# Optimization experiments

Measured on AMD Instinct MI355X. Metric: run time of the kernel, lower is better.

## Reference

```python
import jax, jax.numpy as jnp
import numpy as np
import math

D = 256; B = 4; N = 2048; IN = 16; POS = 3; LAT = 128
DEPTH = 3; RATIO = 0.5; NBLK = 8  # depth*2 + 2 final blocks


def _silu(x):
    return x * jax.nn.sigmoid(x)


def _ln(h, g, b):
    m = h.mean(-1, keepdims=True)
    v = h.var(-1, keepdims=True)  # biased, matches nn.LayerNorm
    return (h - m) / jnp.sqrt(v + 1e-5) * g + b


def _block(h, A, g, b, w1, b1, w2, b2, eps):
    # h: (B, n, D), A: (B, n, n) binary adjacency (block-diag equivalent)
    hn = _ln(h, g, b)
    nb = jnp.einsum('bij,bjd->bid', A, hn)  # sparse.mm(adj, h) per graph
    t = (1.0 + eps) * hn + nb
    t = _silu(t @ w1 + b1) @ w2 + b2
    return h + t


def _forward(x, adj, pos, in_w, in_b, pw1, pb1, pw2, pb2,
             bg, bb, bw1, bb1, bw2, bb2, beps, pool_p, lw, lb, batch_size):
    Bsz = batch_size
    n = adj.shape[0]
    d = in_w.shape[1]
    h = x @ in_w + in_b  # (B*N, D)
    # positional embedding: tile, normalize (unbiased std like torch), MLP
    pt = jnp.tile(pos, (Bsz, 1))
    pn = (pt - pt.mean(0, keepdims=True)) / (pt.std(0, ddof=1, keepdims=True) + 1e-8)
    pe = _silu(pn @ pw1 + pb1) @ pw2 + pb2
    h = (h + pe).reshape(Bsz, n, d)
    A = jnp.broadcast_to(adj, (Bsz, n, n))  # shared block-diag tiles
    blk = 0
    for dep in range(DEPTH):
        for _ in range(2):  # blocks_per_stage
            h = _block(h, A, bg[blk], bb[blk], bw1[blk], bb1[blk],
                       bw2[blk], bb2[blk], beps[blk])
            blk += 1
        # TopKPool: projection score, per-graph top-k, tanh gating
        p = pool_p[dep]
        score = h @ p / jnp.linalg.norm(p)  # (B, n)
        k = int(math.ceil(RATIO * h.shape[1]))  # static
        idx = jnp.sort(jax.lax.top_k(score, k)[1], axis=-1)  # (B, k)
        gate = jnp.tanh(jnp.take_along_axis(score, idx, axis=1))
        h = jnp.take_along_axis(h, idx[:, :, None], axis=1) * gate[:, :, None]
        # subgraph_coo + to_binary: adj[idx][:, idx] per graph
        A = jax.vmap(lambda a, i: a[i][:, i])(A, idx)
        A = (A > 0).astype(h.dtype)
    for _ in range(2):  # final_stage
        h = _block(h, A, bg[blk], bb[blk], bw1[blk], bb1[blk],
                   bw2[blk], bb2[blk], beps[blk])
        blk += 1
    hm = h.mean(1)
    hs = h.std(1, ddof=1) + 1e-6  # torch .std is unbiased
    return jnp.concatenate([hm, hs], axis=-1) @ lw + lb  # (B, LAT)


def setup_inputs() -> dict:
    key = jax.random.key(0)
    ks = jax.random.split(key, 12)
    f32 = jnp.float32
    s = 1.0 / np.sqrt(D)
    x = jax.random.normal(ks[0], (B * N, IN), f32)
    adj = (jax.random.uniform(ks[1], (N, N)) < 0.004).astype(f32)  # ~8 nbrs/node
    pos = jax.random.normal(ks[2], (N, POS), f32)
    return {
        'x': x, 'adj': adj, 'pos': pos,
        'in_w': jax.random.normal(ks[3], (IN, D), f32) / np.sqrt(IN),
        'in_b': jnp.zeros(D, f32),
        'pw1': jax.random.normal(ks[4], (POS, D), f32) / np.sqrt(POS),
        'pb1': jnp.zeros(D, f32),
        'pw2': jax.random.normal(ks[5], (D, D), f32) * s,
        'pb2': jnp.zeros(D, f32),
        'bg': jnp.ones((NBLK, D), f32),
        'bb': jnp.zeros((NBLK, D), f32),
        'bw1': jax.random.normal(ks[6], (NBLK, D, D), f32) * s,
        'bb1': jnp.zeros((NBLK, D), f32),
        'bw2': jax.random.normal(ks[7], (NBLK, D, D), f32) * (0.5 * s),
        'bb2': jnp.zeros((NBLK, D), f32),
        'beps': jnp.zeros(NBLK, f32),
        'pool_p': jax.random.normal(ks[8], (DEPTH, D), f32) * s,
        'lw': jax.random.normal(ks[9], (2 * D, LAT), f32) / np.sqrt(2 * D),
        'lb': jnp.zeros(LAT, f32),
        'batch_size': B,
    }


def reference(x, adj, pos, in_w, in_b, pw1, pb1, pw2, pb2,
              bg, bb, bw1, bb1, bw2, bb2, beps, pool_p, lw, lb, batch_size):
    return _forward(x, adj, pos, in_w, in_b, pw1, pb1, pw2, pb2,
                    bg, bb, bw1, bb1, bw2, bb2, beps, pool_p, lw, lb, batch_size)
```

## Files before the change

kernel.cpp:

```cpp
#include <hip/hip_runtime.h>
#include <hip/hip_bf16.h>

#define NTOT 2048
#define DD 256
#define BSZ 4

typedef _Float16 half_t;
typedef __attribute__((ext_vector_type(8))) _Float16 halfx8;
typedef __attribute__((ext_vector_type(4))) _Float16 halfx4;
typedef __attribute__((ext_vector_type(4))) float f32x4;

__device__ __forceinline__ float blockReduceSum256(float v) {
    __shared__ float red[4];
    for (int off = 32; off > 0; off >>= 1) v += __shfl_down(v, off);
    int lane = threadIdx.x & 63, w = threadIdx.x >> 6;
    __syncthreads();
    if (lane == 0) red[w] = v;
    __syncthreads();
    return red[0] + red[1] + red[2] + red[3];
}

#define SB_WPREP 4352
#define SB_STAT  4356
#define SB_A2L   4868
#define SB_MAPS  4900
__global__ void __launch_bounds__(256) setup_kernel(
    const float* __restrict__ bw1, const float* __restrict__ bw2,
    const float* __restrict__ pw2, half_t* __restrict__ Wt,
    const float* __restrict__ pos, float* __restrict__ pstats,
    const float* __restrict__ poolp, float* __restrict__ pinv,
    const float* __restrict__ adj, int* __restrict__ ldeg0, int* __restrict__ lcol0,
    int* __restrict__ orig, int* __restrict__ inv) {
    int bid = blockIdx.x, tid = threadIdx.x;
    if (bid < SB_WPREP) {
        int m = bid >> 8, rem = bid & 255;
        int nb = (rem >> 4) * 16, kb = (rem & 15) * 16;
        const float* W = (m < 8) ? (bw1 + (size_t)m * DD * DD)
                      : (m < 16) ? (bw2 + (size_t)(m - 8) * DD * DD)
                                 : pw2;
        __shared__ float s[16][17];
        int i = tid >> 4, j = tid & 15;
        s[i][j] = W[(size_t)(kb + i) * DD + nb + j];
        __syncthreads();
        Wt[(size_t)m * DD * DD + (size_t)(nb + i) * DD + kb + j] = (half_t)s[j][i];
    } else if (bid < SB_STAT) {
        int which = bid - SB_WPREP;
        if (which == 0) {
            float s[3] = {0.f, 0.f, 0.f};
            for (int i = tid; i < NTOT; i += 256)
                for (int c = 0; c < 3; ++c) s[c] += pos[i * 3 + c];
            float m[3];
            for (int c = 0; c < 3; ++c) m[c] = blockReduceSum256(s[c]) / (float)NTOT;
            float q[3] = {0.f, 0.f, 0.f};
            for (int i = tid; i < NTOT; i += 256)
                for (int c = 0; c < 3; ++c) { float d = pos[i * 3 + c] - m[c]; q[c] += d * d; }
            for (int c = 0; c < 3; ++c) {
                float t = blockReduceSum256(q[c]);
                if (tid == 0) {
                    float var = ((float)BSZ * t) / ((float)BSZ * NTOT - 1.0f);
                    pstats[c] = m[c];
                    pstats[3 + c] = 1.0f / (sqrtf(var) + 1e-8f);
                }
            }
        } else {
            int dep = which - 1;
            float v = poolp[dep * DD + tid];
            float ss = blockReduceSum256(v * v);
            if (tid == 0) pinv[dep] = rsqrtf(ss);
        }
    } else if (bid < SB_A2L) {
        int row = (bid - SB_STAT) * 4 + (tid >> 6);
        int lane = tid & 63;
        int run = 0;
        for (int j0 = 0; j0 < NTOT; j0 += 64) {
            int j = j0 + lane;
            bool pred = adj[(size_t)row * NTOT + j] != 0.f;
            unsigned long long mask = __ballot(pred);
            if (pred) {
                int pos2 = run + __popcll(mask & ((1ull << lane) - 1ull));
                if (pos2 < 64) lcol0[row * 64 + pos2] = j;
            }
            run += __popcll(mask);
        }
        if (lane == 0) ldeg0[row] = run < 64 ? run : 64;
    } else {
        int t = (bid - SB_A2L) * 256 + tid;
        int i = t & (NTOT - 1);
        orig[t] = i; inv[t] = i;
    }
}

__global__ void __launch_bounds__(256) pe_h_kernel(
    const float* __restrict__ pos, const float* __restrict__ pstats,
    const float* __restrict__ pw1, const float* __restrict__ pb1,
    const half_t* __restrict__ Wt16, const float* __restrict__ pb2,
    const float* __restrict__ x, const float* __restrict__ in_w,
    const float* __restrict__ in_b, float* __restrict__ h, float* __restrict__ z) {
    __shared__ half_t tb[16][264];
    __shared__ float iw[16][DD];
    __shared__ float xs[16][16];
    __shared__ float part[4][16][2];
    __shared__ float mrs[16][2];
    int tid = threadIdx.x;
    int i0 = blockIdx.x * 16;
    {
        int rl = tid >> 4, cb = (tid & 15) * 16;
        float pn[3];
#pragma unroll
        for (int c = 0; c < 3; ++c)
            pn[c] = (pos[(i0 + rl) * 3 + c] - pstats[c]) * pstats[3 + c];
#pragma unroll
        for (int u = 0; u < 16; ++u) {
            int d = cb + u;
            float a = pb1[d];
            a += pn[0] * pw1[d];
            a += pn[1] * pw1[DD + d];
            a += pn[2] * pw1[2 * DD + d];
            a = a / (1.0f + expf(-a));
            tb[rl][d] = (half_t)a;
        }
        int k = tid >> 4;
#pragma unroll
        for (int u = 0; u < 16; ++u) iw[k][cb + u] = in_w[k * DD + cb + u];
    }
    __syncthreads();
    int w = tid >> 6, l = tid & 63;
    int lo = l & 15, hi = l >> 4;
    int kb = hi * 8;
    float pe_r[4][4];
    {
        f32x4 acc[4] = {};
#pragma unroll
        for (int k0 = 0; k0 < DD; k0 += 32) {
            halfx8 a0 = *(const halfx8*)&tb[lo][kb + k0];
#pragma unroll
            for (int j = 0; j < 4; ++j) {
                halfx8 bj = *(const halfx8*)(Wt16 + (size_t)(w * 64 + j * 16 + lo) * DD + kb + k0);
                acc[j] = __builtin_amdgcn_mfma_f32_16x16x32_f16(a0, bj, acc[j], 0, 0, 0);
            }
        }
#pragma unroll
        for (int j = 0; j < 4; ++j) {
            float bs = pb2[w * 64 + j * 16 + lo];
#pragma unroll
            for (int q = 0; q < 4; ++q) pe_r[j][q] = acc[j][q] + bs;
        }
    }
    float xb[4];
#pragma unroll
    for (int j = 0; j < 4; ++j) xb[j] = in_b[w * 64 + j * 16 + lo];
    for (int b = 0; b < BSZ; ++b) {
        __syncthreads();
        xs[tid >> 4][tid & 15] = x[(size_t)(b * NTOT + i0 + (tid >> 4)) * 16 + (tid & 15)];
        __syncthreads();
        float vh[4][4];
#pragma unroll
        for (int q = 0; q < 4; ++q) {
            int rl = hi * 4 + q;
            float s = 0.f, ss = 0.f;
#pragma unroll
            for (int j = 0; j < 4; ++j) {
                int c = w * 64 + j * 16 + lo;
                float acc = xb[j];
#pragma unroll
                for (int k = 0; k < 16; ++k) acc += xs[rl][k] * iw[k][c];
                float v = acc + pe_r[j][q];
                vh[j][q] = v;
                s += v; ss += v * v;
            }
#pragma unroll
            for (int m = 1; m < 16; m <<= 1) { s += __shfl_xor(s, m); ss += __shfl_xor(ss, m); }
            if (lo == 0) { part[w][rl][0] = s; part[w][rl][1] = ss; }
        }
        __syncthreads();
        if (tid < 16) {
            float s = 0.f, ss = 0.f;
#pragma unroll
            for (int w2 = 0; w2 < 4; ++w2) { s += part[w2][tid][0]; ss += part[w2][tid][1]; }
            float mean = s * (1.0f / DD);
            float var = ss * (1.0f / DD) - mean * mean;
            mrs[tid][0] = mean;
            mrs[tid][1] = rsqrtf(var + 1e-5f);
        }
        __syncthreads();
#pragma unroll
        for (int q = 0; q < 4; ++q) {
            int rl = hi * 4 + q;
            size_t r = (size_t)(b * NTOT + i0 + rl);
            float mean = mrs[rl][0], rs = mrs[rl][1];
#pragma unroll
            for (int j = 0; j < 4; ++j) {
                int c = w * 64 + j * 16 + lo;
                float v = vh[j][q];
                h[r * DD + c] = v;
                z[r * DD + c] = (v - mean) * rs;
            }
        }
    }
}

template <int SCORE>
__global__ void __launch_bounds__(256) layer_kernel(
    float* __restrict__ h, const float* __restrict__ zin, float* __restrict__ zout,
    const half_t* __restrict__ Wt1, const half_t* __restrict__ Wt2,
    const float* __restrict__ b1v, const float* __restrict__ b2v,
    const float* __restrict__ gv, const float* __restrict__ bbv,
    const float* __restrict__ beps, int blk,
    const int* __restrict__ ldeg0, const int* __restrict__ lcol0,
    const int* __restrict__ orig, const int* __restrict__ inv,
    const float* __restrict__ poolp, const float* __restrict__ pinv_all,
    float* __restrict__ scores, int dep, int n, int tag) {
    __shared__ half_t tb[16][264];
    __shared__ half_t ub[16][264];
    __shared__ float part[4][16][3];
    __shared__ float mrs[16][2];
    int tid = threadIdx.x;
    int rowBase = blockIdx.x * 16;
    float eps1 = 1.0f + beps[blk];

    {
        int rl = tid >> 4, cg = tid & 15;
        int r = rowBase + rl;
        int b = r / n, i = r - b * n;
        const f32x4* zb = (const f32x4*)zin + (size_t)b * n * 64;
        f32x4 acc[4];
#pragma unroll
        for (int u = 0; u < 4; ++u) acc[u] = zb[(size_t)i * 64 + cg + 16 * u] * eps1;
        int cnt = 0;
        if (tag == 0) {
            int deg = ldeg0[i];
            const int* lc = lcol0 + i * 64;
            int p = 0;
            for (; p + 4 <= deg; p += 4) {
                int j0 = lc[p], j1 = lc[p + 1], j2 = lc[p + 2], j3 = lc[p + 3];
#pragma unroll
                for (int u = 0; u < 4; ++u) {
                    f32x4 v0 = zb[(size_t)j0 * 64 + cg + 16 * u];
                    f32x4 v1 = zb[(size_t)j1 * 64 + cg + 16 * u];
                    f32x4 v2 = zb[(size_t)j2 * 64 + cg + 16 * u];
                    f32x4 v3 = zb[(size_t)j3 * 64 + cg + 16 * u];
                    acc[u] += (v0 + v1) + (v2 + v3);
                }
            }
            for (; p < deg; ++p) {
                int j = lc[p];
#pragma unroll
                for (int u = 0; u < 4; ++u) acc[u] += zb[(size_t)j * 64 + cg + 16 * u];
            }
            cnt = deg;
        } else {
            int o = orig[b * NTOT + i];
            int deg = ldeg0[o];
            const int* lc = lcol0 + o * 64;
            const int* invb = inv + b * NTOT;
            int p = 0;
            for (; p + 4 <= deg; p += 4) {
                int c0 = lc[p], c1 = lc[p + 1], c2 = lc[p + 2], c3 = lc[p + 3];
                int v0 = invb[c0], v1 = invb[c1], v2 = invb[c2], v3 = invb[c3];
                if ((v0 >> 12) == tag) {
                    int j = v0 & 4095; ++cnt;
#pragma unroll
                    for (int u = 0; u < 4; ++u) acc[u] += zb[(size_t)j * 64 + cg + 16 * u];
                }
                if ((v1 >> 12) == tag) {
                    int j = v1 & 4095; ++cnt;
#pragma unroll
                    for (int u = 0; u < 4; ++u) acc[u] += zb[(size_t)j * 64 + cg + 16 * u];
                }
                if ((v2 >> 12) == tag) {
                    int j = v2 & 4095; ++cnt;
#pragma unroll
                    for (int u = 0; u < 4; ++u) acc[u] += zb[(size_t)j * 64 + cg + 16 * u];
                }
                if ((v3 >> 12) == tag) {
                    int j = v3 & 4095; ++cnt;
#pragma unroll
                    for (int u = 0; u < 4; ++u) acc[u] += zb[(size_t)j * 64 + cg + 16 * u];
                }
            }
            for (; p < deg; ++p) {
                int v = invb[lc[p]];
                if ((v >> 12) == tag) {
                    int j = v & 4095; ++cnt;
#pragma unroll
                    for (int u = 0; u < 4; ++u) acc[u] += zb[(size_t)j * 64 + cg + 16 * u];
                }
            }
        }
        float coefb = eps1 + (float)cnt;
#pragma unroll
        for (int u = 0; u < 4; ++u) {
            int c4 = cg + 16 * u;
            f32x4 gvv = ((const f32x4*)gv)[c4];
            f32x4 bvv = ((const f32x4*)bbv)[c4];
            f32x4 tv = gvv * acc[u] + bvv * coefb;
            halfx4 th;
#pragma unroll
            for (int e = 0; e < 4; ++e) th[e] = (half_t)tv[e];
            *(halfx4*)&tb[rl][c4 * 4] = th;
        }
    }
    __syncthreads();

    int w = tid >> 6, l = tid & 63;
    int lo = l & 15, hi = l >> 4;
    int kb = hi * 8;

    {
        f32x4 acc[4] = {};
#pragma unroll
        for (int k0 = 0; k0 < DD; k0 += 32) {
            halfx8 a0 = *(const halfx8*)&tb[lo][kb + k0];
#pragma unroll
            for (int j = 0; j < 4; ++j) {
                halfx8 bj = *(const halfx8*)(Wt1 + (size_t)(w * 64 + j * 16 + lo) * DD + kb + k0);
                acc[j] = __builtin_amdgcn_mfma_f32_16x16x32_f16(a0, bj, acc[j], 0, 0, 0);
            }
        }
        float bs[4];
#pragma unroll
        for (int j = 0; j < 4; ++j) bs[j] = b1v[w * 64 + j * 16 + lo];
#pragma unroll
        for (int q = 0; q < 4; ++q)
#pragma unroll
            for (int j = 0; j < 4; ++j) {
                float v = acc[j][q] + bs[j];
                v = v / (1.0f + expf(-v));
                ub[hi * 4 + q][w * 64 + j * 16 + lo] = (half_t)v;
            }
    }
    __syncthreads();

    {
        f32x4 acc[4] = {};
#pragma unroll
        for (int k0 = 0; k0 < DD; k0 += 32) {
            halfx8 a0 = *(const halfx8*)&ub[lo][kb + k0];
#pragma unroll
            for (int j = 0; j < 4; ++j) {
                halfx8 bj = *(const halfx8*)(Wt2 + (size_t)(w * 64 + j * 16 + lo) * DD + kb + k0);
                acc[j] = __builtin_amdgcn_mfma_f32_16x16x32_f16(a0, bj, acc[j], 0, 0, 0);
            }
        }
        float bs[4], pv[4] = {};
#pragma unroll
        for (int j = 0; j < 4; ++j) bs[j] = b2v[w * 64 + j * 16 + lo];
        if (SCORE) {
#pragma unroll
            for (int j = 0; j < 4; ++j) pv[j] = poolp[dep * DD + w * 64 + j * 16 + lo];
        }
        float vh[4][4];
#pragma unroll
        for (int q = 0; q < 4; ++q) {
            int r = rowBase + hi * 4 + q;
            float s = 0.f, ss = 0.f, sp = 0.f;
#pragma unroll
            for (int j = 0; j < 4; ++j) {
                int c = w * 64 + j * 16 + lo;
                float v = h[(size_t)r * DD + c] + acc[j][q] + bs[j];
                vh[j][q] = v;
                s += v; ss += v * v;
                if (SCORE) sp += v * pv[j];
            }
#pragma unroll
            for (int m = 1; m < 16; m <<= 1) {
                s += __shfl_xor(s, m); ss += __shfl_xor(ss, m);
                if (SCORE) sp += __shfl_xor(sp, m);
            }
            if (lo == 0) {
                int rl = hi * 4 + q;
                part[w][rl][0] = s; part[w][rl][1] = ss;
                if (SCORE) part[w][rl][2] = sp;
            }
        }
        __syncthreads();
        if (tid < 16) {
            float s = 0.f, ss = 0.f, sp = 0.f;
#pragma unroll
            for (int w2 = 0; w2 < 4; ++w2) {
                s += part[w2][tid][0]; ss += part[w2][tid][1];
                if (SCORE) sp += part[w2][tid][2];
            }
            float mean = s * (1.0f / DD);
            float var = ss * (1.0f / DD) - mean * mean;
            mrs[tid][0] = mean;
            mrs[tid][1] = rsqrtf(var + 1e-5f);
            if (SCORE) {
                int r = rowBase + tid;
                int b2 = r / n, ii = r - b2 * n;
                scores[b2 * NTOT + ii] = sp * pinv_all[dep];
            }
        }
        __syncthreads();
#pragma unroll
        for (int q = 0; q < 4; ++q) {
            int rl = hi * 4 + q;
            int r = rowBase + rl;
            float mean = mrs[rl][0], rs = mrs[rl][1];
#pragma unroll
            for (int j = 0; j < 4; ++j) {
                int c = w * 64 + j * 16 + lo;
                float v = vh[j][q];
                h[(size_t)r * DD + c] = v;
                zout[(size_t)r * DD + c] = (v - mean) * rs;
            }
        }
    }
}

__global__ void topk_kernel(const float* __restrict__ scores, const int* __restrict__ orig_cur,
                            int* __restrict__ orig_next, int* __restrict__ idx_local,
                            float* __restrict__ gate, int n, int k) {
    __shared__ unsigned keys[2048];
    __shared__ int hist[256];
    __shared__ int sg[256], se[256];
    __shared__ int sh_bucket, sh_r, sh_cnt;
    __shared__ unsigned cand[256];
    __shared__ unsigned sh_thr;
    int b = blockIdx.x;
    const float* sc = scores + b * NTOT;
    int tid = threadIdx.x;
    for (int i = tid; i < n; i += 256) {
        unsigned u = __float_as_uint(sc[i]);
        keys[i] = (u & 0x80000000u) ? ~u : (u | 0x80000000u);
    }
    hist[tid] = 0;
    if (tid == 0) sh_cnt = 0;
    __syncthreads();
    for (int i = tid; i < n; i += 256) atomicAdd(&hist[keys[i] >> 24], 1);
    __syncthreads();
    int cnt = hist[tid];
    sg[tid] = cnt;
    __syncthreads();
    for (int off = 1; off < 256; off <<= 1) {
        int v = (tid >= off) ? sg[tid - off] : 0;
        __syncthreads();
        sg[tid] += v;
        __syncthreads();
    }
    int r = n - k;
    int incl = sg[tid], excl = incl - cnt;
    if (excl <= r && r < incl) { sh_bucket = tid; sh_r = r - excl; }
    __syncthreads();
    int b1 = sh_bucket, r1 = sh_r;
    int c = hist[b1];
    unsigned thrkey;
    if (c <= 256) {
        for (int i = tid; i < n; i += 256) {
            unsigned key = keys[i];
            if ((key >> 24) == (unsigned)b1) {
                int pos = atomicAdd(&sh_cnt, 1);
                cand[pos] = key;
            }
        }
        __syncthreads();
        if (tid < c) {
            unsigned mine = cand[tid];
            int less = 0, eq = 0;
            for (int j = 0; j < c; ++j) {
                unsigned oth = cand[j];
                less += (oth < mine); eq += (oth == mine);
            }
            if (less <= r1 && r1 < less + eq) sh_thr = mine;
        }
        __syncthreads();
        thrkey = sh_thr;
    } else {
        unsigned prefix = ((unsigned)b1) << 24;
        int rr = r1;
        for (int shift = 16; shift >= 0; shift -= 8) {
            __syncthreads();
            hist[tid] = 0;
            __syncthreads();
            unsigned mask = 0xFFFFFFFFu << (shift + 8);
            for (int i = tid; i < n; i += 256) {
                unsigned key = keys[i];
                if ((key & mask) == (prefix & mask)) atomicAdd(&hist[(key >> shift) & 255], 1);
            }
            __syncthreads();
            int cnt2 = hist[tid];
            sg[tid] = cnt2;
            __syncthreads();
            for (int off = 1; off < 256; off <<= 1) {
                int v = (tid >= off) ? sg[tid - off] : 0;
                __syncthreads();
                sg[tid] += v;
                __syncthreads();
            }
            int incl2 = sg[tid], excl2 = incl2 - cnt2;
            if (excl2 <= rr && rr < incl2) { sh_bucket = tid; sh_r = rr - excl2; }
            __syncthreads();
            prefix |= ((unsigned)sh_bucket) << shift;
            rr = sh_r;
            __syncthreads();
        }
        thrkey = prefix;
    }
    unsigned uthr = (thrkey & 0x80000000u) ? (thrkey ^ 0x80000000u) : ~thrkey;
    float thr = __uint_as_float(uthr);
    int chunk = n / 256;
    int base = tid * chunk;
    int cgt = 0, ceq = 0;
    for (int u = 0; u < chunk; ++u) {
        float s = sc[base + u];
        cgt += (s > thr); ceq += (s == thr);
    }
    sg[tid] = cgt; se[tid] = ceq; __syncthreads();
    for (int off = 1; off < 256; off <<= 1) {
        int vg = (tid >= off) ? sg[tid - off] : 0;
        int ve = (tid >= off) ? se[tid - off] : 0;
        __syncthreads();
        sg[tid] += vg; se[tid] += ve;
        __syncthreads();
    }
    int total_gt = sg[255];
    int ties = k - total_gt;
    int gtb = sg[tid] - cgt, eqb = se[tid] - ceq;
    for (int u = 0; u < chunk; ++u) {
        int i = base + u;
        float s = sc[i];
        bool isgt = (s > thr), iseq = (s == thr);
        bool keep = isgt || (iseq && eqb < ties);
        if (keep) {
            int pos = gtb + (eqb < ties ? eqb : ties);
            idx_local[b * NTOT + pos] = i;
            gate[b * NTOT + pos] = tanhf(s);
            orig_next[b * NTOT + pos] = orig_cur[b * NTOT + i];
        }
        gtb += isgt; eqb += iseq;
    }
}

__global__ void __launch_bounds__(64) gather_kernel(
    const float* __restrict__ h, const int* __restrict__ idx_local,
    const float* __restrict__ gate, const int* __restrict__ orig_new,
    float* __restrict__ hout, float* __restrict__ zout, int* __restrict__ inv,
    int n_old, int k, int tag) {
    int r = blockIdx.x;
    int b = r / k, rr = r - b * k;
    int lane = threadIdx.x;
    int src = idx_local[b * NTOT + rr];
    float gg = gate[b * NTOT + rr];
    f32x4 v = ((const f32x4*)h)[(size_t)(b * n_old + src) * 64 + lane] * gg;
    ((f32x4*)hout)[(size_t)r * 64 + lane] = v;
    float s = v[0] + v[1] + v[2] + v[3];
    float ss = v[0] * v[0] + v[1] * v[1] + v[2] * v[2] + v[3] * v[3];
#pragma unroll
    for (int m = 1; m < 64; m <<= 1) { s += __shfl_xor(s, m); ss += __shfl_xor(ss, m); }
    float mean = s * (1.0f / DD);
    float rs = rsqrtf(ss * (1.0f / DD) - mean * mean + 1e-5f);
    f32x4 zv = (v - mean) * rs;
    ((f32x4*)zout)[(size_t)r * 64 + lane] = zv;
    if (lane == 0) inv[b * NTOT + orig_new[b * NTOT + rr]] = (tag << 12) | rr;
}

__global__ void __launch_bounds__(256) readout_final_kernel(
    const float* __restrict__ h, const float* __restrict__ lw,
    const float* __restrict__ lb, float* __restrict__ out) {
    __shared__ float feat[512];
    int b = blockIdx.x, d = threadIdx.x;
    const float* hb = h + (size_t)b * 256 * DD;
    float s = 0.f;
    for (int i = 0; i < 256; ++i) s += hb[(size_t)i * DD + d];
    float mean = s / 256.0f;
    float s2 = 0.f;
    for (int i = 0; i < 256; ++i) {
        float diff = hb[(size_t)i * DD + d] - mean;
        s2 += diff * diff;
    }
    feat[d] = mean;
    feat[256 + d] = sqrtf(s2 / 255.0f) + 1e-6f;
    __syncthreads();
    if (d < 128) {
        float acc = lb[d];
        for (int k = 0; k < 512; ++k) acc += feat[k] * lw[k * 128 + d];
        out[b * 128 + d] = acc;
    }
}

extern "C" void kernel_launch(void* const* d_in, const int* in_sizes, int n_in,
                              void* d_out, int out_size, void* d_ws, size_t ws_size,
                              hipStream_t stream) {
    (void)in_sizes; (void)n_in; (void)out_size; (void)ws_size;
    const float* x     = (const float*)d_in[0];
    const float* adj   = (const float*)d_in[1];
    const float* pos   = (const float*)d_in[2];
    const float* in_w  = (const float*)d_in[3];
    const float* in_b  = (const float*)d_in[4];
    const float* pw1   = (const float*)d_in[5];
    const float* pb1   = (const float*)d_in[6];
    const float* pw2   = (const float*)d_in[7];
    const float* pb2   = (const float*)d_in[8];
    const float* bg    = (const float*)d_in[9];
    const float* bb    = (const float*)d_in[10];
    const float* bw1   = (const float*)d_in[11];
    const float* bb1   = (const float*)d_in[12];
    const float* bw2   = (const float*)d_in[13];
    const float* bb2   = (const float*)d_in[14];
    const float* beps  = (const float*)d_in[15];
    const float* poolp = (const float*)d_in[16];
    const float* lw    = (const float*)d_in[17];
    const float* lb    = (const float*)d_in[18];
    float* out = (float*)d_out;

    char* wp = (char*)d_ws;
    auto alloc = [&](size_t bytes) -> void* {
        void* p = (void*)wp;
        wp += (bytes + 255) & ~(size_t)255;
        return p;
    };
    const size_t HBYTES = (size_t)BSZ * NTOT * DD * sizeof(float);
    float*  h    = (float*)alloc(HBYTES);
    float*  bufC = (float*)alloc(HBYTES);
    float*  zA   = (float*)alloc(HBYTES);
    float*  zB   = (float*)alloc(HBYTES);
    half_t* Wt   = (half_t*)alloc((size_t)17 * DD * DD * sizeof(half_t));
    float* pstats  = (float*)alloc(8 * sizeof(float));
    float* pinv    = (float*)alloc(4 * sizeof(float));
    float* scores  = (float*)alloc(BSZ * NTOT * sizeof(float));
    float* gate    = (float*)alloc(BSZ * NTOT * sizeof(float));
    int*   origA   = (int*)alloc(BSZ * NTOT * sizeof(int));
    int*   origB   = (int*)alloc(BSZ * NTOT * sizeof(int));
    int*   idxl    = (int*)alloc(BSZ * NTOT * sizeof(int));
    int*   inv     = (int*)alloc(BSZ * NTOT * sizeof(int));
    int*   ldeg0   = (int*)alloc(NTOT * sizeof(int));
    int*   lcol0   = (int*)alloc((size_t)NTOT * 64 * sizeof(int));

    setup_kernel<<<SB_MAPS, 256, 0, stream>>>(bw1, bw2, pw2, Wt, pos, pstats, poolp, pinv,
                                              adj, ldeg0, lcol0, origA, inv);
    pe_h_kernel<<<NTOT / 16, 256, 0, stream>>>(pos, pstats, pw1, pb1,
                                               Wt + (size_t)16 * DD * DD, pb2,
                                               x, in_w, in_b, h, zA);

    float* hcur = h;
    float* halt = bufC;
    float* zin = zA;
    float* zout = zB;
    int* orig = origA;
    int* orign = origB;
    int n = NTOT;
    int blk = 0;
    for (int dep = 0; dep < 4; ++dep) {
        for (int s = 0; s < 2; ++s) {
            int rows = BSZ * n;
            if (s == 1 && dep < 3) {
                layer_kernel<1><<<rows / 16, 256, 0, stream>>>(
                    hcur, zin, zout, Wt + (size_t)blk * DD * DD, Wt + (size_t)(8 + blk) * DD * DD,
                    bb1 + blk * DD, bb2 + blk * DD, bg + blk * DD, bb + blk * DD,
                    beps, blk, ldeg0, lcol0, orig, inv, poolp, pinv, scores, dep, n, dep);
            } else {
                layer_kernel<0><<<rows / 16, 256, 0, stream>>>(
                    hcur, zin, zout, Wt + (size_t)blk * DD * DD, Wt + (size_t)(8 + blk) * DD * DD,
                    bb1 + blk * DD, bb2 + blk * DD, bg + blk * DD, bb + blk * DD,
                    beps, blk, ldeg0, lcol0, orig, inv, nullptr, nullptr, nullptr, 0, n, dep);
            }
            { float* t = zin; zin = zout; zout = t; }
            ++blk;
        }
        if (dep < 3) {
            int k = n / 2;
            topk_kernel<<<BSZ, 256, 0, stream>>>(scores, orig, orign, idxl, gate, n, k);
            { int* t = orig; orig = orign; orign = t; }
            gather_kernel<<<BSZ * k, 64, 0, stream>>>(hcur, idxl, gate, orig, halt, zin, inv,
                                                      n, k, dep + 1);
            { float* t = hcur; hcur = halt; halt = t; }
            n = k;
        }
    }
    readout_final_kernel<<<BSZ, 256, 0, stream>>>(hcur, lw, lb, out);
}
```

Before: 283.3 us.

## Split sparse aggregation from MLP into separate kernels for large stages

For the first two depth stages (larger graphs), the fused layer kernel is replaced by two kernels. A wave-per-row aggregation kernel gathers neighbor rows and writes the LayerNorm-affine result as fp16 to a new buffer, and a separate MFMA MLP kernel reads that buffer. This gives the irregular gather much more parallelism (rows/4 blocks, one row per wave) and removes gather stalls from the GEMM blocks. The cost is an extra launch per layer and an fp16 intermediate round trip through global memory. Smaller later stages keep the fused kernel.

```diff
diff --git a/kernel.cpp b/kernel.cpp
--- a/kernel.cpp
+++ b/kernel.cpp
@@ -199,6 +199,181 @@
     }
 }
 
+__global__ void __launch_bounds__(256) agg_kernel(
+    const float* __restrict__ zin, half_t* __restrict__ tb,
+    const float* __restrict__ gv, const float* __restrict__ bbv,
+    const float* __restrict__ beps, int blk,
+    const int* __restrict__ ldeg0, const int* __restrict__ lcol0,
+    const int* __restrict__ orig, const int* __restrict__ inv, int n, int tag) {
+    int w = threadIdx.x >> 6, lane = threadIdx.x & 63;
+    int r = blockIdx.x * 4 + w;
+    int b = r / n, i = r - b * n;
+    float eps1 = 1.0f + beps[blk];
+    const f32x4* zb = (const f32x4*)zin + (size_t)b * n * 64;
+    f32x4 acc = zb[(size_t)i * 64 + lane] * eps1;
+    int cnt = 0;
+    if (tag == 0) {
+        int deg = ldeg0[i];
+        const int* lc = lcol0 + i * 64;
+        int p = 0;
+        for (; p + 4 <= deg; p += 4) {
+            int j0 = lc[p], j1 = lc[p + 1], j2 = lc[p + 2], j3 = lc[p + 3];
+            f32x4 v0 = zb[(size_t)j0 * 64 + lane];
+            f32x4 v1 = zb[(size_t)j1 * 64 + lane];
+            f32x4 v2 = zb[(size_t)j2 * 64 + lane];
+            f32x4 v3 = zb[(size_t)j3 * 64 + lane];
+            acc += (v0 + v1) + (v2 + v3);
+        }
+        for (; p < deg; ++p) acc += zb[(size_t)lc[p] * 64 + lane];
+        cnt = deg;
+    } else {
+        int o = orig[b * NTOT + i];
+        int deg = ldeg0[o];
+        const int* lc = lcol0 + o * 64;
+        const int* invb = inv + b * NTOT;
+        int p = 0;
+        for (; p + 4 <= deg; p += 4) {
+            int v0 = invb[lc[p]], v1 = invb[lc[p + 1]];
+            int v2 = invb[lc[p + 2]], v3 = invb[lc[p + 3]];
+            if ((v0 >> 12) == tag) { acc += zb[(size_t)(v0 & 4095) * 64 + lane]; ++cnt; }
+            if ((v1 >> 12) == tag) { acc += zb[(size_t)(v1 & 4095) * 64 + lane]; ++cnt; }
+            if ((v2 >> 12) == tag) { acc += zb[(size_t)(v2 & 4095) * 64 + lane]; ++cnt; }
+            if ((v3 >> 12) == tag) { acc += zb[(size_t)(v3 & 4095) * 64 + lane]; ++cnt; }
+        }
+        for (; p < deg; ++p) {
+            int v = invb[lc[p]];
+            if ((v >> 12) == tag) { acc += zb[(size_t)(v & 4095) * 64 + lane]; ++cnt; }
+        }
+    }
+    float coefb = eps1 + (float)cnt;
+    f32x4 gvv = ((const f32x4*)gv)[lane];
+    f32x4 bvv = ((const f32x4*)bbv)[lane];
+    f32x4 tv = gvv * acc + bvv * coefb;
+    halfx4 th;
+#pragma unroll
+    for (int e = 0; e < 4; ++e) th[e] = (half_t)tv[e];
+    ((halfx4*)tb)[(size_t)r * 64 + lane] = th;
+}
+
+template <int SCORE>
+__global__ void __launch_bounds__(256) mlp_kernel(
+    float* __restrict__ h, const half_t* __restrict__ tbg, float* __restrict__ zout,
+    const half_t* __restrict__ Wt1, const half_t* __restrict__ Wt2,
+    const float* __restrict__ b1v, const float* __restrict__ b2v,
+    const float* __restrict__ poolp, const float* __restrict__ pinv_all,
+    float* __restrict__ scores, int dep, int n) {
+    __shared__ half_t ub[16][264];
+    __shared__ float part[4][16][3];
+    __shared__ float mrs[16][2];
+    int tid = threadIdx.x;
+    int rowBase = blockIdx.x * 16;
+    int w = tid >> 6, l = tid & 63;
+    int lo = l & 15, hi = l >> 4;
+    int kb = hi * 8;
+
+    {
+        const half_t* a0p = tbg + (size_t)(rowBase + lo) * DD + kb;
+        f32x4 acc[4] = {};
+#pragma unroll
+        for (int k0 = 0; k0 < DD; k0 += 32) {
+            halfx8 a0 = *(const halfx8*)(a0p + k0);
+#pragma unroll
+            for (int j = 0; j < 4; ++j) {
+                halfx8 bj = *(const halfx8*)(Wt1 + (size_t)(w * 64 + j * 16 + lo) * DD + kb + k0);
+                acc[j] = __builtin_amdgcn_mfma_f32_16x16x32_f16(a0, bj, acc[j], 0, 0, 0);
+            }
+        }
+        float bs[4];
+#pragma unroll
+        for (int j = 0; j < 4; ++j) bs[j] = b1v[w * 64 + j * 16 + lo];
+#pragma unroll
+        for (int q = 0; q < 4; ++q)
+#pragma unroll
+            for (int j = 0; j < 4; ++j) {
+                float v = acc[j][q] + bs[j];
+                v = v / (1.0f + expf(-v));
+                ub[hi * 4 + q][w * 64 + j * 16 + lo] = (half_t)v;
+            }
+    }
+    __syncthreads();
+
+    {
+        f32x4 acc[4] = {};
+#pragma unroll
+        for (int k0 = 0; k0 < DD; k0 += 32) {
+            halfx8 a0 = *(const halfx8*)&ub[lo][kb + k0];
+#pragma unroll
+            for (int j = 0; j < 4; ++j) {
+                halfx8 bj = *(const halfx8*)(Wt2 + (size_t)(w * 64 + j * 16 + lo) * DD + kb + k0);
+                acc[j] = __builtin_amdgcn_mfma_f32_16x16x32_f16(a0, bj, acc[j], 0, 0, 0);
+            }
+        }
+        float bs[4], pv[4] = {};
+#pragma unroll
+        for (int j = 0; j < 4; ++j) bs[j] = b2v[w * 64 + j * 16 + lo];
+        if (SCORE) {
+#pragma unroll
+            for (int j = 0; j < 4; ++j) pv[j] = poolp[dep * DD + w * 64 + j * 16 + lo];
+        }
+        float vh[4][4];
+#pragma unroll
+        for (int q = 0; q < 4; ++q) {
+            int r = rowBase + hi * 4 + q;
+            float s = 0.f, ss = 0.f, sp = 0.f;
+#pragma unroll
+            for (int j = 0; j < 4; ++j) {
+                int c = w * 64 + j * 16 + lo;
+                float v = h[(size_t)r * DD + c] + acc[j][q] + bs[j];
+                vh[j][q] = v;
+                s += v; ss += v * v;
+                if (SCORE) sp += v * pv[j];
+            }
+#pragma unroll
+            for (int m = 1; m < 16; m <<= 1) {
+                s += __shfl_xor(s, m); ss += __shfl_xor(ss, m);
+                if (SCORE) sp += __shfl_xor(sp, m);
+            }
+            if (lo == 0) {
+                int rl = hi * 4 + q;
+                part[w][rl][0] = s; part[w][rl][1] = ss;
+                if (SCORE) part[w][rl][2] = sp;
+            }
+        }
+        __syncthreads();
+        if (tid < 16) {
+            float s = 0.f, ss = 0.f, sp = 0.f;
+#pragma unroll
+            for (int w2 = 0; w2 < 4; ++w2) {
+                s += part[w2][tid][0]; ss += part[w2][tid][1];
+                if (SCORE) sp += part[w2][tid][2];
+            }
+            float mean = s * (1.0f / DD);
+            float var = ss * (1.0f / DD) - mean * mean;
+            mrs[tid][0] = mean;
+            mrs[tid][1] = rsqrtf(var + 1e-5f);
+            if (SCORE) {
+                int r = rowBase + tid;
+                int b2 = r / n, ii = r - b2 * n;
+                scores[b2 * NTOT + ii] = sp * pinv_all[dep];
+            }
+        }
+        __syncthreads();
+#pragma unroll
+        for (int q = 0; q < 4; ++q) {
+            int rl = hi * 4 + q;
+            int r = rowBase + rl;
+            float mean = mrs[rl][0], rs = mrs[rl][1];
+#pragma unroll
+            for (int j = 0; j < 4; ++j) {
+                int c = w * 64 + j * 16 + lo;
+                float v = vh[j][q];
+                h[(size_t)r * DD + c] = v;
+                zout[(size_t)r * DD + c] = (v - mean) * rs;
+            }
+        }
+    }
+}
+
 template <int SCORE>
 __global__ void __launch_bounds__(256) layer_kernel(
     float* __restrict__ h, const float* __restrict__ zin, float* __restrict__ zout,
@@ -255,8 +430,8 @@
             const int* invb = inv + b * NTOT;
             int p = 0;
             for (; p + 4 <= deg; p += 4) {
-                int c0 = lc[p], c1 = lc[p + 1], c2 = lc[p + 2], c3 = lc[p + 3];
-                int v0 = invb[c0], v1 = invb[c1], v2 = invb[c2], v3 = invb[c3];
+                int v0 = invb[lc[p]], v1 = invb[lc[p + 1]];
+                int v2 = invb[lc[p + 2]], v3 = invb[lc[p + 3]];
                 if ((v0 >> 12) == tag) {
                     int j = v0 & 4095; ++cnt;
 #pragma unroll
@@ -614,6 +789,7 @@
     float*  bufC = (float*)alloc(HBYTES);
     float*  zA   = (float*)alloc(HBYTES);
     float*  zB   = (float*)alloc(HBYTES);
+    half_t* tbg  = (half_t*)alloc(HBYTES / 2);
     half_t* Wt   = (half_t*)alloc((size_t)17 * DD * DD * sizeof(half_t));
     float* pstats  = (float*)alloc(8 * sizeof(float));
     float* pinv    = (float*)alloc(4 * sizeof(float));
@@ -643,16 +819,27 @@
     for (int dep = 0; dep < 4; ++dep) {
         for (int s = 0; s < 2; ++s) {
             int rows = BSZ * n;
-            if (s == 1 && dep < 3) {
-                layer_kernel<1><<<rows / 16, 256, 0, stream>>>(
-                    hcur, zin, zout, Wt + (size_t)blk * DD * DD, Wt + (size_t)(8 + blk) * DD * DD,
-                    bb1 + blk * DD, bb2 + blk * DD, bg + blk * DD, bb + blk * DD,
-                    beps, blk, ldeg0, lcol0, orig, inv, poolp, pinv, scores, dep, n, dep);
+            const half_t* W1 = Wt + (size_t)blk * DD * DD;
+            const half_t* W2 = Wt + (size_t)(8 + blk) * DD * DD;
+            const float* B1 = bb1 + blk * DD;
+            const float* B2 = bb2 + blk * DD;
+            const float* G  = bg + blk * DD;
+            const float* BB = bb + blk * DD;
+            int sc = (s == 1 && dep < 3) ? 1 : 0;
+            if (dep < 2) {
+                agg_kernel<<<rows / 4, 256, 0, stream>>>(
+                    zin, tbg, G, BB, beps, blk, ldeg0, lcol0, orig, inv, n, dep);
+                if (sc) mlp_kernel<1><<<rows / 16, 256, 0, stream>>>(
+                    hcur, tbg, zout, W1, W2, B1, B2, poolp, pinv, scores, dep, n);
+                else    mlp_kernel<0><<<rows / 16, 256, 0, stream>>>(
+                    hcur, tbg, zout, W1, W2, B1, B2, nullptr, nullptr, nullptr, 0, n);
             } else {
-                layer_kernel<0><<<rows / 16, 256, 0, stream>>>(
-                    hcur, zin, zout, Wt + (size_t)blk * DD * DD, Wt + (size_t)(8 + blk) * DD * DD,
-                    bb1 + blk * DD, bb2 + blk * DD, bg + blk * DD, bb + blk * DD,
-                    beps, blk, ldeg0, lcol0, orig, inv, nullptr, nullptr, nullptr, 0, n, dep);
+                if (sc) layer_kernel<1><<<rows / 16, 256, 0, stream>>>(
+                    hcur, zin, zout, W1, W2, B1, B2, G, BB, beps, blk,
+                    ldeg0, lcol0, orig, inv, poolp, pinv, scores, dep, n, dep);
+                else    layer_kernel<0><<<rows / 16, 256, 0, stream>>>(
+                    hcur, zin, zout, W1, W2, B1, B2, G, BB, beps, blk,
+                    ldeg0, lcol0, orig, inv, nullptr, nullptr, nullptr, 0, n, dep);
             }
             { float* t = zin; zin = zout; zout = t; }
             ++blk;
```

Result: slower. 293.5 us (+3.6%).
